# Performance work log

Measured on AMD Instinct MI355X. Metric: run time of the kernel, lower is better.

## Reference

```python
import jax, jax.numpy as jnp
import numpy as np

DIM = 1024
B, K = 8192, 16


def setup_inputs() -> dict:
    key = jax.random.key(0)
    ks = jax.random.split(key, 7)
    # xavier_uniform bound for square [C,C]: sqrt(6/(C+C))
    bq = float(np.sqrt(6.0 / (DIM + DIM)))
    ba_bound = float(np.sqrt(6.0 / (DIM + 1)))
    return {
        "query": jax.random.normal(ks[0], (B, DIM), dtype=jnp.float32),
        "key": jax.random.normal(ks[1], (B, K, DIM), dtype=jnp.float32),
        "value": jax.random.normal(ks[2], (B, K, DIM), dtype=jnp.float32),
        "Wq": jax.random.uniform(ks[3], (DIM, DIM), jnp.float32, -bq, bq),
        "Wk": jax.random.uniform(ks[4], (DIM, DIM), jnp.float32, -bq, bq),
        "Wa": jax.random.uniform(ks[5], (1, DIM), jnp.float32, -ba_bound, ba_bound),
        "ba": jnp.ones((1,), dtype=jnp.float32),
    }


def reference(query, key, value, Wq, Wk, Wa, ba):
    # query: [B, C]; key/value: [B, K, C]
    C = query.shape[-1]
    res = query
    q = query[:, None, :]                       # [B, 1, C]
    k = jnp.concatenate([q, key], axis=1)       # [B, K+1, C] (query prepended)
    v = jnp.concatenate([q, value], axis=1)     # [B, K+1, C]
    qp = q @ Wq.T                               # [B, 1, C]
    kp = k @ Wk.T                               # [B, K+1, C]
    scale = 1.0 / jnp.sqrt(jnp.asarray(C, dtype=jnp.float32))
    scores = jnp.einsum('bqc,bkc->bqk', qp, kp) * scale   # [B, 1, K+1]
    attn_w = jax.nn.softmax(scores, axis=-1)
    attn = jnp.einsum('bqk,bkc->bqc', attn_w, v)[:, 0, :]  # [B, C]
    alpha = jax.nn.sigmoid(res @ Wa.T + ba)     # [B, 1]
    out = res + alpha * attn                    # gated residual
    # F.normalize(p=2, dim=-1, eps=1e-12)
    norm = jnp.linalg.norm(out, axis=-1, keepdims=True)
    return out / jnp.maximum(norm, 1e-12)
```

## Files before the change

kernel.cpp:

```cpp
#include <hip/hip_runtime.h>
#include <hip/hip_bf16.h>

#define DIM   1024
#define BATCH 8192
#define KV    16

typedef __attribute__((ext_vector_type(4))) float f32x4;
typedef __attribute__((ext_vector_type(8))) short short8;

static __device__ __forceinline__ unsigned short f2bf(float x) {
  return __builtin_bit_cast(unsigned short, __float2bfloat16(x));
}
static __device__ __forceinline__ float bf2f(unsigned short x) {
  return __bfloat162float(__builtin_bit_cast(__hip_bfloat16, x));
}
static __device__ __forceinline__ float dot4(f32x4 a, f32x4 b) {
  return a.x * b.x + a.y * b.y + a.z * b.z + a.w * b.w;
}

static __device__ __forceinline__ void gl_lds16(const unsigned short* g, unsigned short* l) {
  __builtin_amdgcn_global_load_lds(
      (const __attribute__((address_space(1))) void*)g,
      (__attribute__((address_space(3))) void*)l, 16, 0, 0);
}

__global__ __launch_bounds__(256) void convert_q(const f32x4* __restrict__ in,
                                                 ushort4* __restrict__ out, int n4) {
  int i = blockIdx.x * blockDim.x + threadIdx.x;
  int stride = gridDim.x * blockDim.x;
  for (; i < n4; i += stride) {
    f32x4 f = in[i];
    ushort4 o;
    o.x = f2bf(f.x); o.y = f2bf(f.y); o.z = f2bf(f.z); o.w = f2bf(f.w);
    out[i] = o;
  }
}

__global__ __launch_bounds__(256) void transpose_w(const float* __restrict__ Wq,
                                                   const float* __restrict__ Wk,
                                                   unsigned short* __restrict__ WqT,
                                                   unsigned short* __restrict__ WkT) {
  __shared__ float tile[32][33];
  const float* src = blockIdx.z ? Wk : Wq;
  unsigned short* dst = blockIdx.z ? WkT : WqT;
  int x = blockIdx.x * 32 + threadIdx.x;
  int y0 = blockIdx.y * 32;
  #pragma unroll
  for (int i = threadIdx.y; i < 32; i += 8)
    tile[i][threadIdx.x] = src[(size_t)(y0 + i) * DIM + x];
  __syncthreads();
  int x2 = blockIdx.y * 32 + threadIdx.x;
  int y2 = blockIdx.x * 32;
  #pragma unroll
  for (int i = threadIdx.y; i < 32; i += 8)
    dst[(size_t)(y2 + i) * DIM + x2] = f2bf(tile[threadIdx.x][i]);
}

__global__ __launch_bounds__(256) void gemm_nt64(const unsigned short* __restrict__ A,
                                                 const unsigned short* __restrict__ B,
                                                 unsigned short* __restrict__ C,
                                                 int N, int K) {
  __shared__ __align__(16) unsigned short As[64 * 32];
  __shared__ __align__(16) unsigned short Bs[64 * 32];
  const int tid = threadIdx.x;
  const int lane = tid & 63;
  const int wave = tid >> 6;
  const int wr = wave >> 1, wc = wave & 1;
  const size_t bm = (size_t)blockIdx.x * 64;
  const size_t bn = (size_t)blockIdx.y * 64;

  f32x4 acc[2][2];
  #pragma unroll
  for (int m = 0; m < 2; ++m)
    #pragma unroll
    for (int n = 0; n < 2; ++n)
      acc[m][n] = (f32x4){0.f, 0.f, 0.f, 0.f};

  const int r0 = tid >> 2;
  const int cc = (tid & 3) * 8;
  const int kg = lane >> 4;
  const int rowf = lane & 15;

  for (int kt = 0; kt < K; kt += 32) {
    gl_lds16(A + (bm + r0) * K + kt + cc, As + tid * 8);
    gl_lds16(B + (bn + r0) * K + kt + cc, Bs + tid * 8);
    __syncthreads();
    short8 af[2], bfr[2];
    #pragma unroll
    for (int m = 0; m < 2; ++m)
      af[m] = *(const short8*)(As + ((wr * 32 + m * 16 + rowf) * 32 + kg * 8));
    #pragma unroll
    for (int n = 0; n < 2; ++n)
      bfr[n] = *(const short8*)(Bs + ((wc * 32 + n * 16 + rowf) * 32 + kg * 8));
    #pragma unroll
    for (int m = 0; m < 2; ++m)
      #pragma unroll
      for (int n = 0; n < 2; ++n)
        acc[m][n] = __builtin_amdgcn_mfma_f32_16x16x32_bf16(af[m], bfr[n], acc[m][n], 0, 0, 0);
    __syncthreads();
  }

  const int rq = (lane >> 4) * 4;
  const int colf = lane & 15;
  #pragma unroll
  for (int m = 0; m < 2; ++m)
    #pragma unroll
    for (int n = 0; n < 2; ++n)
      #pragma unroll
      for (int i = 0; i < 4; ++i)
        C[(bm + wr * 32 + m * 16 + rq + i) * N + bn + wc * 32 + n * 16 + colf] =
            f2bf(acc[m][n][i]);
}

__global__ __launch_bounds__(256) void gemm_u(const unsigned short* __restrict__ A,
                                              const unsigned short* __restrict__ B,
                                              unsigned short* __restrict__ C,
                                              int K, int ntN, int ldc) {
  const int cpx = gridDim.x >> 3;
  const int wg = (blockIdx.x & 7) * cpx + (blockIdx.x >> 3);
  const size_t bm = (size_t)(wg / ntN) * 128;
  const size_t bn = (size_t)(wg % ntN) * 128;

  __shared__ __align__(16) unsigned short As[128 * 32];
  __shared__ __align__(16) unsigned short Bs[128 * 32];
  const int tid = threadIdx.x;
  const int lane = tid & 63;
  const int wave = tid >> 6;
  const int wr = wave >> 1, wc = wave & 1;

  f32x4 acc[4][4];
  #pragma unroll
  for (int m = 0; m < 4; ++m)
    #pragma unroll
    for (int n = 0; n < 4; ++n)
      acc[m][n] = (f32x4){0.f, 0.f, 0.f, 0.f};

  const int r0 = tid >> 2;
  const int r1 = 64 + (tid >> 2);
  const int cc = (tid & 3) * 8;
  const int kg = lane >> 4;
  const int rowf = lane & 15;

  for (int kt = 0; kt < K; kt += 32) {
    gl_lds16(A + (bm + r0) * K + kt + cc, As + tid * 8);
    gl_lds16(A + (bm + r1) * K + kt + cc, As + 2048 + tid * 8);
    gl_lds16(B + (bn + r0) * K + kt + cc, Bs + tid * 8);
    gl_lds16(B + (bn + r1) * K + kt + cc, Bs + 2048 + tid * 8);
    __syncthreads();
    short8 af[4], bfr[4];
    #pragma unroll
    for (int m = 0; m < 4; ++m)
      af[m] = *(const short8*)(As + ((wr * 64 + m * 16 + rowf) * 32 + kg * 8));
    #pragma unroll
    for (int n = 0; n < 4; ++n)
      bfr[n] = *(const short8*)(Bs + ((wc * 64 + n * 16 + rowf) * 32 + kg * 8));
    #pragma unroll
    for (int m = 0; m < 4; ++m)
      #pragma unroll
      for (int n = 0; n < 4; ++n)
        acc[m][n] = __builtin_amdgcn_mfma_f32_16x16x32_bf16(af[m], bfr[n], acc[m][n], 0, 0, 0);
    __syncthreads();
  }

  const int rq = (lane >> 4) * 4;
  const int colf = lane & 15;
  #pragma unroll
  for (int m = 0; m < 4; ++m)
    #pragma unroll
    for (int n = 0; n < 4; ++n)
      #pragma unroll
      for (int i = 0; i < 4; ++i) {
        size_t row = bm + wr * 64 + m * 16 + rq + i;
        size_t col = bn + wc * 64 + n * 16 + colf;
        C[row * (size_t)ldc + col] = f2bf(acc[m][n][i]);
      }
}

__global__ __launch_bounds__(256) void epilogue(const float* __restrict__ query,
                                                const float* __restrict__ key,
                                                const float* __restrict__ value,
                                                const float* __restrict__ Wa,
                                                const float* __restrict__ ba,
                                                const unsigned short* __restrict__ u,
                                                float* __restrict__ out) {
  const int b = blockIdx.x;
  const int tid = threadIdx.x;
  const int lane = tid & 63, wave = tid >> 6;
  const f32x4* q4 = (const f32x4*)(query + (size_t)b * DIM);
  const f32x4* k4 = (const f32x4*)(key + (size_t)b * KV * DIM);
  const f32x4* v4 = (const f32x4*)(value + (size_t)b * KV * DIM);

  f32x4 qv = q4[tid];
  ushort4 ub = ((const ushort4*)(u + (size_t)b * 2048))[tid];
  f32x4 uv;
  uv.x = bf2f(ub.x); uv.y = bf2f(ub.y); uv.z = bf2f(ub.z); uv.w = bf2f(ub.w);
  f32x4 wv = ((const f32x4*)Wa)[tid];

  float s[17];
  s[0] = dot4(qv, uv);
  float ad = dot4(qv, wv);
  #pragma unroll
  for (int j = 1; j <= 16; ++j) {
    f32x4 kv = __builtin_nontemporal_load(k4 + (j - 1) * 256 + tid);
    s[j] = dot4(uv, kv);
  }

  f32x4 vv[16];
  #pragma unroll
  for (int j = 0; j < 16; ++j)
    vv[j] = __builtin_nontemporal_load(v4 + j * 256 + tid);

  #pragma unroll
  for (int m = 32; m >= 1; m >>= 1) {
    #pragma unroll
    for (int j = 0; j < 17; ++j) s[j] += __shfl_xor(s[j], m);
    ad += __shfl_xor(ad, m);
  }
  __shared__ float red[4][18];
  if (lane == 0) {
    #pragma unroll
    for (int j = 0; j < 17; ++j) red[wave][j] = s[j];
    red[wave][17] = ad;
  }
  __syncthreads();

  float wt[17];
  float mx = -1e30f;
  #pragma unroll
  for (int j = 0; j < 17; ++j) {
    float t = (red[0][j] + red[1][j] + red[2][j] + red[3][j]) * 0.03125f;
    wt[j] = t;
    mx = fmaxf(mx, t);
  }
  float den = 0.f;
  #pragma unroll
  for (int j = 0; j < 17; ++j) {
    wt[j] = expf(wt[j] - mx);
    den += wt[j];
  }
  float adt = red[0][17] + red[1][17] + red[2][17] + red[3][17] + ba[0];
  float alpha = 1.0f / (1.0f + expf(-adt));
  float am = alpha / den;

  f32x4 acc = qv * wt[0];
  #pragma unroll
  for (int j = 1; j <= 16; ++j) acc += vv[j - 1] * wt[j];
  f32x4 t = qv + acc * am;

  float ssp = dot4(t, t);
  #pragma unroll
  for (int m = 32; m >= 1; m >>= 1) ssp += __shfl_xor(ssp, m);
  __shared__ float red2[4];
  if (lane == 0) red2[wave] = ssp;
  __syncthreads();
  float nrm = sqrtf(red2[0] + red2[1] + red2[2] + red2[3]);
  float inv = 1.0f / fmaxf(nrm, 1e-12f);

  ((f32x4*)(out + (size_t)b * DIM))[tid] = t * inv;
}

extern "C" void kernel_launch(void* const* d_in, const int* in_sizes, int n_in,
                              void* d_out, int out_size, void* d_ws, size_t ws_size,
                              hipStream_t stream) {
  const float* query = (const float*)d_in[0];
  const float* key   = (const float*)d_in[1];
  const float* value = (const float*)d_in[2];
  const float* Wq    = (const float*)d_in[3];
  const float* Wk    = (const float*)d_in[4];
  const float* Wa    = (const float*)d_in[5];
  const float* ba    = (const float*)d_in[6];

  unsigned short* qbf = (unsigned short*)d_ws;
  unsigned short* WqT = qbf + (size_t)BATCH * DIM;
  unsigned short* WkT = WqT + (size_t)DIM * DIM;
  unsigned short* Mt  = WkT + (size_t)DIM * DIM;
  unsigned short* ubf = (unsigned short*)d_out;

  convert_q<<<2048, 256, 0, stream>>>((const f32x4*)query, (ushort4*)qbf, BATCH * DIM / 4);
  transpose_w<<<dim3(32, 32, 2), dim3(32, 8), 0, stream>>>(Wq, Wk, WqT, WkT);
  gemm_nt64<<<dim3(16, 16), 256, 0, stream>>>(WkT, WqT, Mt, DIM, DIM);
  gemm_u<<<512, 256, 0, stream>>>(qbf, Mt, ubf, DIM, DIM / 128, 2048);
  epilogue<<<BATCH, 256, 0, stream>>>(query, key, value, Wa, ba, ubf, (float*)d_out);
}
```

Before: 245.6 us.

## Fuse query-projection GEMM and attention epilogue into one LDS-staged kernel

```diff
diff --git a/kernel.cpp b/kernel.cpp
--- a/kernel.cpp
+++ b/kernel.cpp
@@ -4,6 +4,8 @@
 #define DIM   1024
 #define BATCH 8192
 #define KV    16
+#define MB    32
+#define ROWEL 1280
 
 typedef __attribute__((ext_vector_type(4))) float f32x4;
 typedef __attribute__((ext_vector_type(8))) short short8;
@@ -13,9 +15,6 @@
 }
 static __device__ __forceinline__ float bf2f(unsigned short x) {
   return __bfloat162float(__builtin_bit_cast(__hip_bfloat16, x));
-}
-static __device__ __forceinline__ float dot4(f32x4 a, f32x4 b) {
-  return a.x * b.x + a.y * b.y + a.z * b.z + a.w * b.w;
 }
 
 static __device__ __forceinline__ void gl_lds16(const unsigned short* g, unsigned short* l) {
@@ -112,151 +111,162 @@
             f2bf(acc[m][n][i]);
 }
 
-__global__ __launch_bounds__(256) void gemm_u(const unsigned short* __restrict__ A,
-                                              const unsigned short* __restrict__ B,
-                                              unsigned short* __restrict__ C,
-                                              int K, int ntN, int ldc) {
-  const int cpx = gridDim.x >> 3;
-  const int wg = (blockIdx.x & 7) * cpx + (blockIdx.x >> 3);
-  const size_t bm = (size_t)(wg / ntN) * 128;
-  const size_t bn = (size_t)(wg % ntN) * 128;
-
-  __shared__ __align__(16) unsigned short As[128 * 32];
-  __shared__ __align__(16) unsigned short Bs[128 * 32];
+__global__ __launch_bounds__(512, 2) void fused_attn(
+    const unsigned short* __restrict__ qbf,
+    const unsigned short* __restrict__ Mt,
+    const float* __restrict__ key,
+    const float* __restrict__ value,
+    const float* __restrict__ Wa,
+    const float* __restrict__ ba,
+    float* __restrict__ out) {
+  __shared__ __align__(16) unsigned short S[MB * ROWEL];
   const int tid = threadIdx.x;
   const int lane = tid & 63;
   const int wave = tid >> 6;
-  const int wr = wave >> 1, wc = wave & 1;
-
-  f32x4 acc[4][4];
-  #pragma unroll
-  for (int m = 0; m < 4; ++m)
-    #pragma unroll
-    for (int n = 0; n < 4; ++n)
-      acc[m][n] = (f32x4){0.f, 0.f, 0.f, 0.f};
-
-  const int r0 = tid >> 2;
-  const int r1 = 64 + (tid >> 2);
-  const int cc = (tid & 3) * 8;
-  const int kg = lane >> 4;
-  const int rowf = lane & 15;
-
-  for (int kt = 0; kt < K; kt += 32) {
-    gl_lds16(A + (bm + r0) * K + kt + cc, As + tid * 8);
-    gl_lds16(A + (bm + r1) * K + kt + cc, As + 2048 + tid * 8);
-    gl_lds16(B + (bn + r0) * K + kt + cc, Bs + tid * 8);
-    gl_lds16(B + (bn + r1) * K + kt + cc, Bs + 2048 + tid * 8);
+  const size_t b0 = (size_t)blockIdx.x * MB;
+
+  #pragma unroll
+  for (int it = 0; it < 8; ++it) {
+    int et = (it * 512 + tid) * 8;
+    int kt = et >> 10;
+    int idx = et & 1023;
+    int r = idx >> 5;
+    int c = idx & 31;
+    gl_lds16(qbf + (b0 + r) * DIM + kt * 32 + c, S + et);
+  }
+  __syncthreads();
+
+  {
+    const int rowf = lane & 15;
+    const int kg = lane >> 4;
+    f32x4 acc[2][8];
+    #pragma unroll
+    for (int mf = 0; mf < 2; ++mf)
+      #pragma unroll
+      for (int f = 0; f < 8; ++f)
+        acc[mf][f] = (f32x4){0.f, 0.f, 0.f, 0.f};
+
+    const unsigned short* Bbase = Mt + (size_t)(wave * 128 + rowf) * DIM + kg * 8;
+    for (int kt = 0; kt < 32; ++kt) {
+      short8 a0 = *(const short8*)(S + kt * 1024 + rowf * 32 + kg * 8);
+      short8 a1 = *(const short8*)(S + kt * 1024 + (16 + rowf) * 32 + kg * 8);
+      #pragma unroll
+      for (int f = 0; f < 8; ++f) {
+        short8 bf8 = *(const short8*)(Bbase + (size_t)f * 16 * DIM + kt * 32);
+        acc[0][f] = __builtin_amdgcn_mfma_f32_16x16x32_bf16(a0, bf8, acc[0][f], 0, 0, 0);
+        acc[1][f] = __builtin_amdgcn_mfma_f32_16x16x32_bf16(a1, bf8, acc[1][f], 0, 0, 0);
+      }
+    }
     __syncthreads();
-    short8 af[4], bfr[4];
-    #pragma unroll
-    for (int m = 0; m < 4; ++m)
-      af[m] = *(const short8*)(As + ((wr * 64 + m * 16 + rowf) * 32 + kg * 8));
-    #pragma unroll
-    for (int n = 0; n < 4; ++n)
-      bfr[n] = *(const short8*)(Bs + ((wc * 64 + n * 16 + rowf) * 32 + kg * 8));
-    #pragma unroll
-    for (int m = 0; m < 4; ++m)
-      #pragma unroll
-      for (int n = 0; n < 4; ++n)
-        acc[m][n] = __builtin_amdgcn_mfma_f32_16x16x32_bf16(af[m], bfr[n], acc[m][n], 0, 0, 0);
-    __syncthreads();
-  }
-
-  const int rq = (lane >> 4) * 4;
-  const int colf = lane & 15;
-  #pragma unroll
-  for (int m = 0; m < 4; ++m)
-    #pragma unroll
-    for (int n = 0; n < 4; ++n)
-      #pragma unroll
-      for (int i = 0; i < 4; ++i) {
-        size_t row = bm + wr * 64 + m * 16 + rq + i;
-        size_t col = bn + wc * 64 + n * 16 + colf;
-        C[row * (size_t)ldc + col] = f2bf(acc[m][n][i]);
-      }
-}
-
-__global__ __launch_bounds__(256) void epilogue(const float* __restrict__ query,
-                                                const float* __restrict__ key,
-                                                const float* __restrict__ value,
-                                                const float* __restrict__ Wa,
-                                                const float* __restrict__ ba,
-                                                const unsigned short* __restrict__ u,
-                                                float* __restrict__ out) {
-  const int b = blockIdx.x;
-  const int tid = threadIdx.x;
-  const int lane = tid & 63, wave = tid >> 6;
-  const f32x4* q4 = (const f32x4*)(query + (size_t)b * DIM);
-  const f32x4* k4 = (const f32x4*)(key + (size_t)b * KV * DIM);
-  const f32x4* v4 = (const f32x4*)(value + (size_t)b * KV * DIM);
-
-  f32x4 qv = q4[tid];
-  ushort4 ub = ((const ushort4*)(u + (size_t)b * 2048))[tid];
-  f32x4 uv;
-  uv.x = bf2f(ub.x); uv.y = bf2f(ub.y); uv.z = bf2f(ub.z); uv.w = bf2f(ub.w);
-  f32x4 wv = ((const f32x4*)Wa)[tid];
-
-  float s[17];
-  s[0] = dot4(qv, uv);
-  float ad = dot4(qv, wv);
-  #pragma unroll
-  for (int j = 1; j <= 16; ++j) {
-    f32x4 kv = __builtin_nontemporal_load(k4 + (j - 1) * 256 + tid);
-    s[j] = dot4(uv, kv);
-  }
-
-  f32x4 vv[16];
-  #pragma unroll
-  for (int j = 0; j < 16; ++j)
-    vv[j] = __builtin_nontemporal_load(v4 + j * 256 + tid);
-
-  #pragma unroll
-  for (int m = 32; m >= 1; m >>= 1) {
-    #pragma unroll
-    for (int j = 0; j < 17; ++j) s[j] += __shfl_xor(s[j], m);
-    ad += __shfl_xor(ad, m);
-  }
-  __shared__ float red[4][18];
-  if (lane == 0) {
-    #pragma unroll
-    for (int j = 0; j < 17; ++j) red[wave][j] = s[j];
-    red[wave][17] = ad;
+
+    #pragma unroll
+    for (int mf = 0; mf < 2; ++mf)
+      #pragma unroll
+      for (int f = 0; f < 8; ++f) {
+        int c = wave * 128 + f * 16 + rowf;
+        int pos = c + ((c >> 5) << 3);
+        #pragma unroll
+        for (int i = 0; i < 4; ++i)
+          S[(mf * 16 + kg * 4 + i) * ROWEL + pos] = f2bf(acc[mf][f][i]);
+      }
   }
   __syncthreads();
 
-  float wt[17];
-  float mx = -1e30f;
-  #pragma unroll
-  for (int j = 0; j < 17; ++j) {
-    float t = (red[0][j] + red[1][j] + red[2][j] + red[3][j]) * 0.03125f;
-    wt[j] = t;
-    mx = fmaxf(mx, t);
-  }
-  float den = 0.f;
-  #pragma unroll
-  for (int j = 0; j < 17; ++j) {
-    wt[j] = expf(wt[j] - mx);
-    den += wt[j];
-  }
-  float adt = red[0][17] + red[1][17] + red[2][17] + red[3][17] + ba[0];
-  float alpha = 1.0f / (1.0f + expf(-adt));
-  float am = alpha / den;
-
-  f32x4 acc = qv * wt[0];
-  #pragma unroll
-  for (int j = 1; j <= 16; ++j) acc += vv[j - 1] * wt[j];
-  f32x4 t = qv + acc * am;
-
-  float ssp = dot4(t, t);
-  #pragma unroll
-  for (int m = 32; m >= 1; m >>= 1) ssp += __shfl_xor(ssp, m);
-  __shared__ float red2[4];
-  if (lane == 0) red2[wave] = ssp;
-  __syncthreads();
-  float nrm = sqrtf(red2[0] + red2[1] + red2[2] + red2[3]);
-  float inv = 1.0f / fmaxf(nrm, 1e-12f);
-
-  ((f32x4*)(out + (size_t)b * DIM))[tid] = t * inv;
+  float wav[16];
+  #pragma unroll
+  for (int r = 0; r < 4; ++r) {
+    f32x4 w4 = *(const f32x4*)(Wa + r * 256 + lane * 4);
+    wav[r * 4 + 0] = w4.x; wav[r * 4 + 1] = w4.y;
+    wav[r * 4 + 2] = w4.z; wav[r * 4 + 3] = w4.w;
+  }
+  const float ba0 = ba[0];
+
+  for (int g = 0; g < 4; ++g) {
+    const int bl = wave * 4 + g;
+    const size_t b = b0 + bl;
+
+    float qf[16], uu[16];
+    #pragma unroll
+    for (int r = 0; r < 4; ++r) {
+      int d = lane * 4 + r * 256;
+      ushort4 q4v = *(const ushort4*)(qbf + b * DIM + d);
+      int pos = d + ((d >> 5) << 3);
+      ushort4 u4v = *(const ushort4*)(S + bl * ROWEL + pos);
+      qf[r * 4 + 0] = bf2f(q4v.x); qf[r * 4 + 1] = bf2f(q4v.y);
+      qf[r * 4 + 2] = bf2f(q4v.z); qf[r * 4 + 3] = bf2f(q4v.w);
+      uu[r * 4 + 0] = bf2f(u4v.x); uu[r * 4 + 1] = bf2f(u4v.y);
+      uu[r * 4 + 2] = bf2f(u4v.z); uu[r * 4 + 3] = bf2f(u4v.w);
+    }
+
+    float s[17];
+    float t0 = 0.f, ad = 0.f;
+    #pragma unroll
+    for (int i = 0; i < 16; ++i) { t0 += qf[i] * uu[i]; ad += qf[i] * wav[i]; }
+    s[0] = t0;
+
+    const float* krow = key + b * (KV * DIM);
+    #pragma unroll
+    for (int j = 1; j <= 16; ++j) {
+      float a2 = 0.f;
+      #pragma unroll
+      for (int r = 0; r < 4; ++r) {
+        f32x4 kv = __builtin_nontemporal_load(
+            (const f32x4*)(krow + (size_t)(j - 1) * DIM + r * 256) + lane);
+        a2 += kv.x * uu[r * 4] + kv.y * uu[r * 4 + 1] +
+              kv.z * uu[r * 4 + 2] + kv.w * uu[r * 4 + 3];
+      }
+      s[j] = a2;
+    }
+
+    #pragma unroll
+    for (int m = 32; m >= 1; m >>= 1) {
+      #pragma unroll
+      for (int j = 0; j < 17; ++j) s[j] += __shfl_xor(s[j], m);
+      ad += __shfl_xor(ad, m);
+    }
+
+    float mx = -1e30f;
+    #pragma unroll
+    for (int j = 0; j < 17; ++j) { s[j] *= 0.03125f; mx = fmaxf(mx, s[j]); }
+    float den = 0.f;
+    #pragma unroll
+    for (int j = 0; j < 17; ++j) { s[j] = expf(s[j] - mx); den += s[j]; }
+    float alpha = 1.f / (1.f + expf(-(ad + ba0)));
+    float am = alpha / den;
+
+    float off[16];
+    float w0p = 1.f + am * s[0];
+    #pragma unroll
+    for (int i = 0; i < 16; ++i) off[i] = qf[i] * w0p;
+
+    const float* vrow = value + b * (KV * DIM);
+    #pragma unroll
+    for (int j = 1; j <= 16; ++j) {
+      float wj = am * s[j];
+      #pragma unroll
+      for (int r = 0; r < 4; ++r) {
+        f32x4 vv = __builtin_nontemporal_load(
+            (const f32x4*)(vrow + (size_t)(j - 1) * DIM + r * 256) + lane);
+        off[r * 4 + 0] += wj * vv.x; off[r * 4 + 1] += wj * vv.y;
+        off[r * 4 + 2] += wj * vv.z; off[r * 4 + 3] += wj * vv.w;
+      }
+    }
+
+    float nq = 0.f;
+    #pragma unroll
+    for (int i = 0; i < 16; ++i) nq += off[i] * off[i];
+    #pragma unroll
+    for (int m = 32; m >= 1; m >>= 1) nq += __shfl_xor(nq, m);
+    float inv = 1.f / fmaxf(sqrtf(nq), 1e-12f);
+
+    #pragma unroll
+    for (int r = 0; r < 4; ++r) {
+      f32x4 o;
+      o.x = off[r * 4 + 0] * inv; o.y = off[r * 4 + 1] * inv;
+      o.z = off[r * 4 + 2] * inv; o.w = off[r * 4 + 3] * inv;
+      *((f32x4*)(out + b * DIM + r * 256) + lane) = o;
+    }
+  }
 }
 
 extern "C" void kernel_launch(void* const* d_in, const int* in_sizes, int n_in,
@@ -274,11 +284,9 @@
   unsigned short* WqT = qbf + (size_t)BATCH * DIM;
   unsigned short* WkT = WqT + (size_t)DIM * DIM;
   unsigned short* Mt  = WkT + (size_t)DIM * DIM;
-  unsigned short* ubf = (unsigned short*)d_out;
 
   convert_q<<<2048, 256, 0, stream>>>((const f32x4*)query, (ushort4*)qbf, BATCH * DIM / 4);
   transpose_w<<<dim3(32, 32, 2), dim3(32, 8), 0, stream>>>(Wq, Wk, WqT, WkT);
   gemm_nt64<<<dim3(16, 16), 256, 0, stream>>>(WkT, WqT, Mt, DIM, DIM);
-  gemm_u<<<512, 256, 0, stream>>>(qbf, Mt, ubf, DIM, DIM / 128, 2048);
-  epilogue<<<BATCH, 256, 0, stream>>>(query, key, value, Wa, ba, ubf, (float*)d_out);
-}
+  fused_attn<<<BATCH / MB, 512, 0, stream>>>(qbf, Mt, key, value, Wa, ba, (float*)d_out);
+}
```

Result: slower. 316.6 us (+28.9%).

## Fuse key-score dot products into the u GEMM epilogue via atomic score accumulation

Applied to the files above, without the earlier changes.

```diff
diff --git a/kernel.cpp b/kernel.cpp
--- a/kernel.cpp
+++ b/kernel.cpp
@@ -4,6 +4,7 @@
 #define DIM   1024
 #define BATCH 8192
 #define KV    16
+#define SCP   20
 
 typedef __attribute__((ext_vector_type(4))) float f32x4;
 typedef __attribute__((ext_vector_type(8))) short short8;
@@ -25,15 +26,17 @@
 }
 
 __global__ __launch_bounds__(256) void convert_q(const f32x4* __restrict__ in,
-                                                 ushort4* __restrict__ out, int n4) {
+                                                 ushort4* __restrict__ out, int n4,
+                                                 f32x4* __restrict__ zbuf, int nz4) {
   int i = blockIdx.x * blockDim.x + threadIdx.x;
   int stride = gridDim.x * blockDim.x;
-  for (; i < n4; i += stride) {
-    f32x4 f = in[i];
+  for (int k = i; k < n4; k += stride) {
+    f32x4 f = in[k];
     ushort4 o;
     o.x = f2bf(f.x); o.y = f2bf(f.y); o.z = f2bf(f.z); o.w = f2bf(f.w);
-    out[i] = o;
+    out[k] = o;
   }
+  for (int k = i; k < nz4; k += stride) zbuf[k] = (f32x4){0.f, 0.f, 0.f, 0.f};
 }
 
 __global__ __launch_bounds__(256) void transpose_w(const float* __restrict__ Wq,
@@ -112,17 +115,20 @@
             f2bf(acc[m][n][i]);
 }
 
-__global__ __launch_bounds__(256) void gemm_u(const unsigned short* __restrict__ A,
-                                              const unsigned short* __restrict__ B,
-                                              unsigned short* __restrict__ C,
-                                              int K, int ntN, int ldc) {
+__global__ __launch_bounds__(256) void gemm_u_scores(
+    const unsigned short* __restrict__ qbf,
+    const unsigned short* __restrict__ Mt,
+    const float* __restrict__ key,
+    float* __restrict__ scores) {
+  __shared__ __align__(16) unsigned short S[128 * 136];
+  unsigned short* As = S;
+  unsigned short* Bs = S + 4096;
+
   const int cpx = gridDim.x >> 3;
   const int wg = (blockIdx.x & 7) * cpx + (blockIdx.x >> 3);
-  const size_t bm = (size_t)(wg / ntN) * 128;
-  const size_t bn = (size_t)(wg % ntN) * 128;
-
-  __shared__ __align__(16) unsigned short As[128 * 32];
-  __shared__ __align__(16) unsigned short Bs[128 * 32];
+  const size_t bm = (size_t)(wg >> 3) * 128;
+  const size_t bn = (size_t)(wg & 7) * 128;
+
   const int tid = threadIdx.x;
   const int lane = tid & 63;
   const int wave = tid >> 6;
@@ -141,11 +147,11 @@
   const int kg = lane >> 4;
   const int rowf = lane & 15;
 
-  for (int kt = 0; kt < K; kt += 32) {
-    gl_lds16(A + (bm + r0) * K + kt + cc, As + tid * 8);
-    gl_lds16(A + (bm + r1) * K + kt + cc, As + 2048 + tid * 8);
-    gl_lds16(B + (bn + r0) * K + kt + cc, Bs + tid * 8);
-    gl_lds16(B + (bn + r1) * K + kt + cc, Bs + 2048 + tid * 8);
+  for (int kt = 0; kt < DIM; kt += 32) {
+    gl_lds16(qbf + (bm + r0) * DIM + kt + cc, As + tid * 8);
+    gl_lds16(qbf + (bm + r1) * DIM + kt + cc, As + 2048 + tid * 8);
+    gl_lds16(Mt + (bn + r0) * DIM + kt + cc, Bs + tid * 8);
+    gl_lds16(Mt + (bn + r1) * DIM + kt + cc, Bs + 2048 + tid * 8);
     __syncthreads();
     short8 af[4], bfr[4];
     #pragma unroll
@@ -169,92 +175,114 @@
     #pragma unroll
     for (int n = 0; n < 4; ++n)
       #pragma unroll
-      for (int i = 0; i < 4; ++i) {
-        size_t row = bm + wr * 64 + m * 16 + rq + i;
-        size_t col = bn + wc * 64 + n * 16 + colf;
-        C[row * (size_t)ldc + col] = f2bf(acc[m][n][i]);
+      for (int i = 0; i < 4; ++i)
+        S[(wr * 64 + m * 16 + rq + i) * 136 + (wc * 64 + n * 16 + colf)] =
+            f2bf(acc[m][n][i]);
+  __syncthreads();
+
+  const int g8 = lane >> 3;
+  const int l8 = lane & 7;
+  #pragma unroll
+  for (int bi = 0; bi < 4; ++bi) {
+    const int bl = bi * 32 + wave * 8 + g8;
+    const size_t b = bm + bl;
+
+    float uf[16];
+    {
+      const unsigned short* up = S + bl * 136 + l8 * 16;
+      short8 u0 = *(const short8*)up;
+      short8 u1 = *(const short8*)(up + 8);
+      #pragma unroll
+      for (int t = 0; t < 8; ++t) {
+        uf[t]     = bf2f((unsigned short)u0[t]);
+        uf[t + 8] = bf2f((unsigned short)u1[t]);
       }
-}
-
-__global__ __launch_bounds__(256) void epilogue(const float* __restrict__ query,
-                                                const float* __restrict__ key,
+    }
+
+    {
+      const unsigned short* qp = qbf + b * DIM + bn + l8 * 16;
+      short8 q0 = *(const short8*)qp;
+      short8 q1 = *(const short8*)(qp + 8);
+      float d = 0.f;
+      #pragma unroll
+      for (int t = 0; t < 8; ++t)
+        d += uf[t] * bf2f((unsigned short)q0[t]) + uf[t + 8] * bf2f((unsigned short)q1[t]);
+      d += __shfl_xor(d, 1); d += __shfl_xor(d, 2); d += __shfl_xor(d, 4);
+      if (l8 == 0) atomicAdd(&scores[b * SCP], d);
+    }
+
+    const float* kp = key + (b * KV) * DIM + bn + l8 * 16;
+    #pragma unroll
+    for (int j = 1; j <= KV; ++j) {
+      const f32x4* kk = (const f32x4*)(kp + (size_t)(j - 1) * DIM);
+      f32x4 k0 = __builtin_nontemporal_load(kk);
+      f32x4 k1 = __builtin_nontemporal_load(kk + 1);
+      f32x4 k2 = __builtin_nontemporal_load(kk + 2);
+      f32x4 k3 = __builtin_nontemporal_load(kk + 3);
+      float d = uf[0] * k0.x + uf[1] * k0.y + uf[2] * k0.z + uf[3] * k0.w
+              + uf[4] * k1.x + uf[5] * k1.y + uf[6] * k1.z + uf[7] * k1.w
+              + uf[8] * k2.x + uf[9] * k2.y + uf[10] * k2.z + uf[11] * k2.w
+              + uf[12] * k3.x + uf[13] * k3.y + uf[14] * k3.z + uf[15] * k3.w;
+      d += __shfl_xor(d, 1); d += __shfl_xor(d, 2); d += __shfl_xor(d, 4);
+      if (l8 == 0) atomicAdd(&scores[b * SCP + j], d);
+    }
+  }
+}
+
+__global__ __launch_bounds__(256) void epilogue(const unsigned short* __restrict__ qbf,
                                                 const float* __restrict__ value,
                                                 const float* __restrict__ Wa,
                                                 const float* __restrict__ ba,
-                                                const unsigned short* __restrict__ u,
+                                                const float* __restrict__ scores,
                                                 float* __restrict__ out) {
   const int b = blockIdx.x;
   const int tid = threadIdx.x;
   const int lane = tid & 63, wave = tid >> 6;
-  const f32x4* q4 = (const f32x4*)(query + (size_t)b * DIM);
-  const f32x4* k4 = (const f32x4*)(key + (size_t)b * KV * DIM);
-  const f32x4* v4 = (const f32x4*)(value + (size_t)b * KV * DIM);
-
-  f32x4 qv = q4[tid];
-  ushort4 ub = ((const ushort4*)(u + (size_t)b * 2048))[tid];
-  f32x4 uv;
-  uv.x = bf2f(ub.x); uv.y = bf2f(ub.y); uv.z = bf2f(ub.z); uv.w = bf2f(ub.w);
-  f32x4 wv = ((const f32x4*)Wa)[tid];
-
+
+  ushort4 q4 = *(const ushort4*)(qbf + (size_t)b * DIM + tid * 4);
+  f32x4 qf;
+  qf.x = bf2f(q4.x); qf.y = bf2f(q4.y); qf.z = bf2f(q4.z); qf.w = bf2f(q4.w);
+  f32x4 w4 = ((const f32x4*)Wa)[tid];
+
+  const f32x4* v4 = (const f32x4*)(value + (size_t)b * KV * DIM) + tid;
+  f32x4 vv[16];
+  #pragma unroll
+  for (int j = 0; j < 16; ++j)
+    vv[j] = __builtin_nontemporal_load(v4 + j * 256);
+
+  const float* srow = scores + (size_t)b * SCP;
   float s[17];
-  s[0] = dot4(qv, uv);
-  float ad = dot4(qv, wv);
-  #pragma unroll
-  for (int j = 1; j <= 16; ++j) {
-    f32x4 kv = __builtin_nontemporal_load(k4 + (j - 1) * 256 + tid);
-    s[j] = dot4(uv, kv);
-  }
-
-  f32x4 vv[16];
-  #pragma unroll
-  for (int j = 0; j < 16; ++j)
-    vv[j] = __builtin_nontemporal_load(v4 + j * 256 + tid);
-
-  #pragma unroll
-  for (int m = 32; m >= 1; m >>= 1) {
-    #pragma unroll
-    for (int j = 0; j < 17; ++j) s[j] += __shfl_xor(s[j], m);
-    ad += __shfl_xor(ad, m);
-  }
-  __shared__ float red[4][18];
-  if (lane == 0) {
-    #pragma unroll
-    for (int j = 0; j < 17; ++j) red[wave][j] = s[j];
-    red[wave][17] = ad;
-  }
+  #pragma unroll
+  for (int j = 0; j < 17; ++j) s[j] = srow[j];
+
+  float mx = -1e30f;
+  #pragma unroll
+  for (int j = 0; j < 17; ++j) { s[j] *= 0.03125f; mx = fmaxf(mx, s[j]); }
+  float den = 0.f;
+  #pragma unroll
+  for (int j = 0; j < 17; ++j) { s[j] = expf(s[j] - mx); den += s[j]; }
+
+  float ad = dot4(qf, w4);
+  #pragma unroll
+  for (int m = 32; m >= 1; m >>= 1) ad += __shfl_xor(ad, m);
+  __shared__ float rA[4];
+  if (lane == 0) rA[wave] = ad;
   __syncthreads();
-
-  float wt[17];
-  float mx = -1e30f;
-  #pragma unroll
-  for (int j = 0; j < 17; ++j) {
-    float t = (red[0][j] + red[1][j] + red[2][j] + red[3][j]) * 0.03125f;
-    wt[j] = t;
-    mx = fmaxf(mx, t);
-  }
-  float den = 0.f;
-  #pragma unroll
-  for (int j = 0; j < 17; ++j) {
-    wt[j] = expf(wt[j] - mx);
-    den += wt[j];
-  }
-  float adt = red[0][17] + red[1][17] + red[2][17] + red[3][17] + ba[0];
-  float alpha = 1.0f / (1.0f + expf(-adt));
+  float adt = rA[0] + rA[1] + rA[2] + rA[3] + ba[0];
+  float alpha = 1.f / (1.f + expf(-adt));
   float am = alpha / den;
 
-  f32x4 acc = qv * wt[0];
-  #pragma unroll
-  for (int j = 1; j <= 16; ++j) acc += vv[j - 1] * wt[j];
-  f32x4 t = qv + acc * am;
-
-  float ssp = dot4(t, t);
-  #pragma unroll
-  for (int m = 32; m >= 1; m >>= 1) ssp += __shfl_xor(ssp, m);
-  __shared__ float red2[4];
-  if (lane == 0) red2[wave] = ssp;
+  f32x4 t = qf * (1.f + am * s[0]);
+  #pragma unroll
+  for (int j = 1; j <= 16; ++j) t += vv[j - 1] * (am * s[j]);
+
+  float nq = dot4(t, t);
+  #pragma unroll
+  for (int m = 32; m >= 1; m >>= 1) nq += __shfl_xor(nq, m);
+  __shared__ float rB[4];
+  if (lane == 0) rB[wave] = nq;
   __syncthreads();
-  float nrm = sqrtf(red2[0] + red2[1] + red2[2] + red2[3]);
-  float inv = 1.0f / fmaxf(nrm, 1e-12f);
+  float inv = 1.f / fmaxf(sqrtf(rB[0] + rB[1] + rB[2] + rB[3]), 1e-12f);
 
   ((f32x4*)(out + (size_t)b * DIM))[tid] = t * inv;
 }
@@ -274,11 +302,12 @@
   unsigned short* WqT = qbf + (size_t)BATCH * DIM;
   unsigned short* WkT = WqT + (size_t)DIM * DIM;
   unsigned short* Mt  = WkT + (size_t)DIM * DIM;
-  unsigned short* ubf = (unsigned short*)d_out;
-
-  convert_q<<<2048, 256, 0, stream>>>((const f32x4*)query, (ushort4*)qbf, BATCH * DIM / 4);
+  float* scores = (float*)(Mt + (size_t)DIM * DIM);
+
+  convert_q<<<2048, 256, 0, stream>>>((const f32x4*)query, (ushort4*)qbf, BATCH * DIM / 4,
+                                      (f32x4*)scores, BATCH * SCP / 4);
   transpose_w<<<dim3(32, 32, 2), dim3(32, 8), 0, stream>>>(Wq, Wk, WqT, WkT);
   gemm_nt64<<<dim3(16, 16), 256, 0, stream>>>(WkT, WqT, Mt, DIM, DIM);
-  gemm_u<<<512, 256, 0, stream>>>(qbf, Mt, ubf, DIM, DIM / 128, 2048);
-  epilogue<<<BATCH, 256, 0, stream>>>(query, key, value, Wa, ba, ubf, (float*)d_out);
-}
+  gemm_u_scores<<<512, 256, 0, stream>>>(qbf, Mt, key, scores);
+  epilogue<<<BATCH, 256, 0, stream>>>(qbf, value, Wa, ba, scores, (float*)d_out);
+}
```

After: 313.3 us. 27.6% more time.
